# Performance work log

Hardware: AMD Instinct MI355X
Metric: run time of the kernel (lower is better)

Reference implementation:

```python
import jax, jax.numpy as jnp
import numpy as np

B, N, K = 8, 4096, 16
C_IN = 3
MLP = (64, 64, 128)


def _init_conv(key, c_out, c_in):
    kw, kb = jax.random.split(key)
    bound = 1.0 / np.sqrt(c_in)
    W = jax.random.uniform(kw, (c_out, c_in), jnp.float32, -bound, bound)
    b = jax.random.uniform(kb, (c_out,), jnp.float32, -bound, bound)
    return W, b


def setup_inputs() -> dict:
    key = jax.random.key(0)
    k0, k1, k2, k3 = jax.random.split(key, 4)
    xyz = jax.random.normal(k0, (B, C_IN, N), jnp.float32)
    W0, b0 = _init_conv(k1, MLP[0], C_IN)
    W1, b1 = _init_conv(k2, MLP[1], MLP[0])
    W2, b2 = _init_conv(k3, MLP[2], MLP[1])
    return {"xyz": xyz, "W0": W0, "b0": b0, "W1": W1, "b1": b1, "W2": W2, "b2": b2}


def reference(xyz, W0, b0, W1, b1, W2, b2):
    # xyz: [B, 3, N] -> pts: [B, N, 3]
    pts = jnp.transpose(xyz, (0, 2, 1))
    # KNN: squared pairwise distances [B, N, N]
    sq = jnp.sum(pts * pts, axis=-1)  # [B, N]
    d2 = sq[:, :, None] + sq[:, None, :] - 2.0 * jnp.einsum('bnc,bmc->bnm', pts, pts)
    _, idx = jax.lax.top_k(-d2, K)  # [B, N, K] indices of K nearest (incl. self)
    # gather neighbor coords: [B, N, K, 3]
    grouped = jax.vmap(lambda p, i: p[i])(pts, idx)
    # center-relative coordinates
    rel = grouped - pts[:, :, None, :]  # [B, N, K, 3]
    # three 1x1 conv (= per-point linear) + ReLU layers
    h = jax.nn.relu(jnp.einsum('bnkc,oc->bnko', rel, W0) + b0)
    h = jax.nn.relu(jnp.einsum('bnkc,oc->bnko', h, W1) + b1)
    h = jax.nn.relu(jnp.einsum('bnkc,oc->bnko', h, W2) + b2)
    # max over K neighbors -> [B, N, D'] -> [B, D', N]
    out = jnp.max(h, axis=2)
    return jnp.transpose(out, (0, 2, 1))
```

## Files before the change

### kernel.cpp

```cpp
#include <hip/hip_runtime.h>
#include <cstddef>

#define NB   8
#define NPTS 4096
#define KNN  16
#define FCAP 64

typedef _Float16 h2 __attribute__((ext_vector_type(2)));
typedef _Float16 h8 __attribute__((ext_vector_type(8)));
typedef float    f4 __attribute__((ext_vector_type(4)));

static __device__ __forceinline__ h2 pk2(float a, float b) {
    return __builtin_bit_cast(h2, __builtin_amdgcn_cvt_pkrtz(a, b));
}
static __device__ __forceinline__ unsigned bch(h2 v) {
    return __builtin_bit_cast(unsigned, v);
}

#if __has_builtin(__builtin_amdgcn_fmed3f)
static __device__ __forceinline__ float MED3(float a, float b, float c) {
    return __builtin_amdgcn_fmed3f(a, b, c);
}
#else
static __device__ __forceinline__ float MED3(float a, float b, float c) {
    return fmaxf(fminf(a, b), fminf(fmaxf(a, b), c));
}
#endif

static __device__ __forceinline__ float dist2(float4 Q, float4 p) {
    float dot = fmaf(Q.z, p.z, fmaf(Q.y, p.y, Q.x * p.x));
    return fmaf(-2.0f, dot, Q.w + p.w);
}

__global__ __launch_bounds__(256) void prep_kernel(const float* __restrict__ xyz,
                                                   float4* __restrict__ pts4) {
    int i = blockIdx.x * 256 + threadIdx.x;
    int b = i >> 12;
    int n = i & (NPTS - 1);
    const float* base = xyz + (size_t)b * 3 * NPTS;
    float x = base[n];
    float y = base[NPTS + n];
    float z = base[2 * NPTS + n];
    float sq = fmaf(z, z, fmaf(y, y, x * x));
    pts4[i] = make_float4(x, y, z, sq);
}

__global__ __launch_bounds__(1024, 8) void knn_kernel(const float4* __restrict__ pts4,
                                                      int* __restrict__ idxout) {
    __shared__ uint2 Pm[NPTS];
    __shared__ char  sbuf[32768];
    __shared__ float tauv[64];
    __shared__ int   qcnt[64];
    __shared__ unsigned pmaxu, smaxu;

    float*    partials = (float*)sbuf;
    float*    mbuf     = (float*)(sbuf + 16384);
    unsigned* fidx     = (unsigned*)sbuf;
    float*    fdist    = (float*)(sbuf + 16384);

    int tid = threadIdx.x;
    int b   = blockIdx.y;
    const float4* pb = pts4 + (size_t)b * NPTS;

    if (tid == 0) { pmaxu = 0u; smaxu = 0u; }
    __syncthreads();

    {
        float lm = 0.0f, ls = 0.0f;
        for (int j = tid; j < NPTS; j += 1024) {
            float4 p = pb[j];
            lm = fmaxf(lm, fmaxf(fabsf(p.x), fmaxf(fabsf(p.y), fabsf(p.z))));
            ls = fmaxf(ls, p.w);
            h2 lo = { (_Float16)p.x, (_Float16)p.y };
            h2 hi = { (_Float16)p.z, (_Float16)p.w };
            Pm[j].x = bch(lo);
            Pm[j].y = bch(hi);
        }
        atomicMax(&pmaxu, __builtin_bit_cast(unsigned, lm));
        atomicMax(&smaxu, __builtin_bit_cast(unsigned, ls));
    }

    int wave = tid >> 6, lane = tid & 63;
    int qg = wave >> 2;
    int cq = wave & 3;
    int qcol = lane & 15;
    int rg   = lane >> 4;
    int q  = qg * 16 + qcol;
    int nq = (blockIdx.x << 6) + q;
    int cbase = cq * 1024;

    float4 qf = pb[nq];
    float uxf = -2.0f * qf.x, uyf = -2.0f * qf.y, uzf = -2.0f * qf.z;
    _Float16 uxh = (_Float16)uxf, uyh = (_Float16)uyf, uzh = (_Float16)uzf;
    _Float16 uxl = (_Float16)(uxf - (float)uxh);
    _Float16 uyl = (_Float16)(uyf - (float)uyh);
    _Float16 uzl = (_Float16)(uzf - (float)uzh);
    uint4 bu = {0u, 0u, 0u, 0u};
    if (rg == 0) {
        h2 b01 = {uxh, uyh}, b23 = {uzh, (_Float16)1.0f};
        h2 b45 = {uxl, uyl}, b67 = {uzl, (_Float16)0.0f};
        bu.x = bch(b01); bu.y = bch(b23); bu.z = bch(b45); bu.w = bch(b67);
    }
    h8 bq = __builtin_bit_cast(h8, bu);
    __syncthreads();

    {
        float c0 = __builtin_inff(), c1 = c0, c2 = c0, c3 = c0;
#pragma unroll 2
        for (int t = 0; t < 64; ++t) {
            uint4 au = {0u, 0u, 0u, 0u};
            if (rg == 0) {
                uint2 pd = Pm[cbase + t * 16 + qcol];
                au.x = pd.x; au.y = pd.y; au.z = pd.x; au.w = pd.y;
            }
            f4 d = __builtin_amdgcn_mfma_f32_16x16x32_f16(
                __builtin_bit_cast(h8, au), bq, (f4)0.0f, 0, 0, 0);
            float rmin = fminf(fminf(d[0], d[1]), fminf(d[2], d[3]));
            float p0 = c0, p1 = c1, p2 = c2;
            c0 = fminf(p0, rmin);
            c1 = MED3(rmin, p0, c1);
            c2 = MED3(rmin, p1, c2);
            c3 = MED3(rmin, p2, c3);
        }
        int sb = (cq * 4 + rg) * 4;
        partials[(sb + 0) * 64 + q] = c0;
        partials[(sb + 1) * 64 + q] = c1;
        partials[(sb + 2) * 64 + q] = c2;
        partials[(sb + 3) * 64 + q] = c3;
    }
    __syncthreads();

    if (tid < 256) {
        int qq = tid & 63, k = tid >> 6;
        float mb[16];
#pragma unroll
        for (int j = 0; j < 16; ++j) mb[j] = __builtin_inff();
        for (int s = 0; s < 16; ++s) {
            float v = partials[(k * 16 + s) * 64 + qq];
            float prev = mb[0];
            mb[0] = fminf(mb[0], v);
#pragma unroll
            for (int i = 1; i < 16; ++i) {
                float cur = mb[i];
                mb[i] = MED3(v, prev, cur);
                prev = cur;
            }
        }
#pragma unroll
        for (int j = 0; j < 16; ++j) mbuf[(k * 16 + j) * 64 + qq] = mb[j];
    }
    __syncthreads();

    if (tid < 64) {
        float mb[16];
#pragma unroll
        for (int j = 0; j < 16; ++j) mb[j] = __builtin_inff();
        for (int k = 0; k < 4; ++k) {
            for (int j = 0; j < 16; ++j) {
                float v = mbuf[(k * 16 + j) * 64 + tid];
                if (v >= mb[15]) break;
                float prev = mb[0];
                mb[0] = fminf(mb[0], v);
#pragma unroll
                for (int i = 1; i < 16; ++i) {
                    float cur = mb[i];
                    mb[i] = MED3(v, prev, cur);
                    prev = cur;
                }
            }
        }
        float4 q2 = pb[(blockIdx.x << 6) + tid];
        float sumq = fabsf(q2.x) + fabsf(q2.y) + fabsf(q2.z);
        float qn   = sqrtf(q2.w);
        float pmax = __builtin_bit_cast(float, pmaxu);
        float smax = __builtin_bit_cast(float, smaxu);
        const float r11c = 4.8828125e-4f;
        float tau = mb[15];
        float E0  = smax * r11c + 2.0f * sumq * pmax * r11c + 1.0e-3f;
        float rad2 = fmaxf(tau + 2.0f * E0 + q2.w, 0.0f);
        float R   = qn + sqrtf(rad2);
        float Eq  = (R * R + 2.0f * sumq * R) * r11c + 6.0e-4f;
        Eq = fminf(Eq, E0);
        tauv[tid] = tau + 2.0f * Eq;
        qcnt[tid] = 0;
    }
    __syncthreads();

    {
        float tc = tauv[q];
#pragma unroll 2
        for (int t = 0; t < 64; ++t) {
            uint4 au = {0u, 0u, 0u, 0u};
            if (rg == 0) {
                uint2 pd = Pm[cbase + t * 16 + qcol];
                au.x = pd.x; au.y = pd.y; au.z = pd.x; au.w = pd.y;
            }
            f4 d = __builtin_amdgcn_mfma_f32_16x16x32_f16(
                __builtin_bit_cast(h8, au), bq, (f4)0.0f, 0, 0, 0);
            float rmin = fminf(fminf(d[0], d[1]), fminf(d[2], d[3]));
            if (rmin <= tc) {
#pragma unroll
                for (int r = 0; r < 4; ++r) {
                    if (d[r] <= tc) {
                        int pos = atomicAdd(&qcnt[q], 1);
                        if (pos < FCAP) fidx[pos * 64 + q] = (unsigned)(cbase + t * 16 + rg * 4 + r);
                    }
                }
            }
        }
    }
    __syncthreads();

    for (int e = tid; e < FCAP * 64; e += 1024) {
        int j = e >> 6, qq = e & 63;
        int nc = qcnt[qq]; nc = nc > FCAP ? FCAP : nc;
        if (j < nc) {
            float4 Qf = pb[(blockIdx.x << 6) + qq];
            fdist[e] = dist2(Qf, pb[fidx[e]]);
        }
    }
    __syncthreads();

    if (tid < 64) {
        int nqf = (blockIdx.x << 6) + tid;
        float4 Qf = pb[nqf];
        float bd[16]; int bi[16];
#pragma unroll
        for (int j = 0; j < 16; ++j) { bd[j] = __builtin_inff(); bi[j] = 0; }
        int cnt = qcnt[tid];
        if (cnt <= FCAP) {
            for (int j = 0; j < cnt; ++j) {
                float x  = fdist[j * 64 + tid];
                int   xi = (int)fidx[j * 64 + tid];
                if (x < bd[15] || (x == bd[15] && xi < bi[15])) {
#pragma unroll
                    for (int t = 0; t < 16; ++t) {
                        bool c = (x < bd[t]) || (x == bd[t] && xi < bi[t]);
                        float nd = c ? x  : bd[t];
                        int   ni = c ? xi : bi[t];
                        float od = c ? bd[t] : x;
                        int   oi = c ? bi[t] : xi;
                        bd[t] = nd; bi[t] = ni; x = od; xi = oi;
                    }
                }
            }
        } else {
            for (int m = 0; m < NPTS; ++m) {
                float x = dist2(Qf, pb[m]);
                int  xi = m;
                if (x < bd[15] || (x == bd[15] && xi < bi[15])) {
#pragma unroll
                    for (int t = 0; t < 16; ++t) {
                        bool c = (x < bd[t]) || (x == bd[t] && xi < bi[t]);
                        float nd = c ? x  : bd[t];
                        int   ni = c ? xi : bi[t];
                        float od = c ? bd[t] : x;
                        int   oi = c ? bi[t] : xi;
                        bd[t] = nd; bi[t] = ni; x = od; xi = oi;
                    }
                }
            }
        }
        int* op = idxout + ((size_t)b * NPTS + nqf) * KNN;
#pragma unroll
        for (int j = 0; j < 16; ++j) op[j] = bi[j];
    }
}

__global__ __launch_bounds__(256, 2) void mlp_kernel(
    const float4* __restrict__ pts4, const int* __restrict__ idxin,
    const float* __restrict__ W0, const float* __restrict__ b0,
    const float* __restrict__ W1, const float* __restrict__ b1,
    const float* __restrict__ W2, const float* __restrict__ b2,
    float* __restrict__ out) {

    int tid  = threadIdx.x;
    int wave = tid >> 6, lane = tid & 63;
    int g = lane >> 4, i = lane & 15;

    h2 w0x[8], w0y[8], w0z[8], w0b[8];
#pragma unroll
    for (int s = 0; s < 2; ++s)
#pragma unroll
        for (int v = 0; v < 4; ++v) {
            int c0 = 32 * s + 8 * g + 2 * v;
            w0x[s * 4 + v] = pk2(W0[c0 * 3 + 0], W0[c0 * 3 + 3]);
            w0y[s * 4 + v] = pk2(W0[c0 * 3 + 1], W0[c0 * 3 + 4]);
            w0z[s * 4 + v] = pk2(W0[c0 * 3 + 2], W0[c0 * 3 + 5]);
            w0b[s * 4 + v] = pk2(b0[c0], b0[c0 + 1]);
        }
    h2 b1p[8];
#pragma unroll
    for (int s = 0; s < 2; ++s)
#pragma unroll
        for (int v = 0; v < 4; ++v) {
            int c0 = 32 * s + 16 * (v >> 1) + 4 * g + 2 * (v & 1);
            b1p[s * 4 + v] = pk2(b1[c0], b1[c0 + 1]);
        }
    h8 wf1[4][2];
#pragma unroll
    for (int t = 0; t < 4; ++t)
#pragma unroll
        for (int s = 0; s < 2; ++s) {
            const float* p = W1 + (16 * t + i) * 64 + 32 * s + 8 * g;
            h8 f;
#pragma unroll
            for (int j = 0; j < 8; ++j) f[j] = (_Float16)p[j];
            wf1[t][s] = f;
        }
    h8 wf2[8][2];
#pragma unroll
    for (int t = 0; t < 8; ++t)
#pragma unroll
        for (int s = 0; s < 2; ++s) {
            const float* p = W2 + (16 * t + i) * 64;
            h8 f;
#pragma unroll
            for (int j = 0; j < 8; ++j) {
                int vc = 32 * s + 16 * (j >> 2) + 4 * g + (j & 3);
                f[j] = (_Float16)p[vc];
            }
            wf2[t][s] = f;
        }

    int gw = blockIdx.x * 4 + wave;
    int b  = gw >> 8;
    int n0 = (gw & 255) * 16;

    const float4* pb = pts4 + (size_t)b * NPTS;
    float4 q = pb[n0 + i];
    const int* ip = idxin + ((size_t)b * NPTS + n0 + i) * KNN;

    float mx[8][4];
#pragma unroll
    for (int t = 0; t < 8; ++t)
#pragma unroll
        for (int r = 0; r < 4; ++r) mx[t][r] = -3.4e38f;

    for (int it = 0; it < KNN; ++it) {
        int mi = ip[it];
        float4 p = pb[mi];
        float rx = p.x - q.x, ry = p.y - q.y, rz = p.z - q.z;
        h2 rxx = pk2(rx, rx), ryy = pk2(ry, ry), rzz = pk2(rz, rz);

        h8 h0f[2];
#pragma unroll
        for (int s = 0; s < 2; ++s)
#pragma unroll
            for (int v = 0; v < 4; ++v) {
                h2 hh = __builtin_elementwise_fma(w0z[s * 4 + v], rzz,
                         __builtin_elementwise_fma(w0y[s * 4 + v], ryy,
                          __builtin_elementwise_fma(w0x[s * 4 + v], rxx, w0b[s * 4 + v])));
                hh = __builtin_elementwise_max(hh, (h2)(_Float16)0.0f);
                h0f[s][2 * v]     = hh.x;
                h0f[s][2 * v + 1] = hh.y;
            }

        f4 d1[4];
#pragma unroll
        for (int t = 0; t < 4; ++t) {
            d1[t] = (f4)0.0f;
#pragma unroll
            for (int s = 0; s < 2; ++s)
                d1[t] = __builtin_amdgcn_mfma_f32_16x16x32_f16(wf1[t][s], h0f[s], d1[t], 0, 0, 0);
        }

        h8 h1f[2];
#pragma unroll
        for (int s = 0; s < 2; ++s)
#pragma unroll
            for (int v = 0; v < 4; ++v) {
                int t = 2 * s + (v >> 1), r0 = 2 * (v & 1);
                h2 w = pk2(d1[t][r0], d1[t][r0 + 1]);
                w = w + b1p[s * 4 + v];
                w = __builtin_elementwise_max(w, (h2)(_Float16)0.0f);
                h1f[s][2 * v]     = w.x;
                h1f[s][2 * v + 1] = w.y;
            }

#pragma unroll
        for (int t = 0; t < 8; ++t) {
            f4 d2 = (f4)0.0f;
#pragma unroll
            for (int s = 0; s < 2; ++s)
                d2 = __builtin_amdgcn_mfma_f32_16x16x32_f16(wf2[t][s], h1f[s], d2, 0, 0, 0);
#pragma unroll
            for (int r = 0; r < 4; ++r) mx[t][r] = fmaxf(mx[t][r], d2[r]);
        }
    }

    size_t ob = (size_t)b * 128 * NPTS + n0 + i;
#pragma unroll
    for (int t = 0; t < 8; ++t)
#pragma unroll
        for (int r = 0; r < 4; ++r) {
            int chn = 16 * t + 4 * g + r;
            float v = fmaxf(mx[t][r] + b2[chn], 0.0f);
            out[ob + (size_t)chn * NPTS] = v;
        }
}

extern "C" void kernel_launch(void* const* d_in, const int* in_sizes, int n_in,
                              void* d_out, int out_size, void* d_ws, size_t ws_size,
                              hipStream_t stream) {
    (void)in_sizes; (void)n_in; (void)out_size; (void)ws_size;
    const float* xyz = (const float*)d_in[0];
    const float* W0  = (const float*)d_in[1];
    const float* b0  = (const float*)d_in[2];
    const float* W1  = (const float*)d_in[3];
    const float* b1  = (const float*)d_in[4];
    const float* W2  = (const float*)d_in[5];
    const float* b2  = (const float*)d_in[6];
    float* out = (float*)d_out;

    char* ws = (char*)d_ws;
    float4* pts4 = (float4*)ws;
    int*    idxb = (int*)(ws + (size_t)NB * NPTS * sizeof(float4));

    prep_kernel<<<dim3(NB * NPTS / 256), dim3(256), 0, stream>>>(xyz, pts4);
    knn_kernel<<<dim3(NPTS / 64, NB), dim3(1024), 0, stream>>>(pts4, idxb);
    mlp_kernel<<<dim3(512), dim3(256), 0, stream>>>(
        pts4, idxb, W0, b0, W1, b1, W2, b2, out);
}
```

Measured before the change: 118.3 us.

## Switch KNN distance MFMA from 16x16x32 to 32x32x16 tiles

The KNN distance passes now use the 32x32x16 f16 MFMA instead of 16x16x32. Each wave covers 32 queries and 512 candidates in 16 iterations, and the wave-to-query/candidate mapping changes to 2 query groups by 8 candidate chunks. The goal is fewer MFMA issues and fewer loop iterations per candidate. In exchange, each lane carries 16 output registers, runs a wider min-reduction tree, and the filter pass's unrolled atomic checks grow from 4 to 16 per tile, which may raise register pressure and branch divergence.

```diff
diff --git a/kernel.cpp b/kernel.cpp
--- a/kernel.cpp
+++ b/kernel.cpp
@@ -9,6 +9,7 @@
 typedef _Float16 h2 __attribute__((ext_vector_type(2)));
 typedef _Float16 h8 __attribute__((ext_vector_type(8)));
 typedef float    f4 __attribute__((ext_vector_type(4)));
+typedef float    f16f __attribute__((ext_vector_type(16)));
 
 static __device__ __forceinline__ h2 pk2(float a, float b) {
     return __builtin_bit_cast(h2, __builtin_amdgcn_cvt_pkrtz(a, b));
@@ -81,13 +82,13 @@
     }
 
     int wave = tid >> 6, lane = tid & 63;
-    int qg = wave >> 2;
-    int cq = wave & 3;
-    int qcol = lane & 15;
-    int rg   = lane >> 4;
-    int q  = qg * 16 + qcol;
+    int g  = wave >> 3;
+    int c  = wave & 7;
+    int col = lane & 31;
+    int hl  = lane >> 5;
+    int q  = g * 32 + col;
     int nq = (blockIdx.x << 6) + q;
-    int cbase = cq * 1024;
+    int cbase = c * 512;
 
     float4 qf = pb[nq];
     float uxf = -2.0f * qf.x, uyf = -2.0f * qf.y, uzf = -2.0f * qf.z;
@@ -96,7 +97,7 @@
     _Float16 uyl = (_Float16)(uyf - (float)uyh);
     _Float16 uzl = (_Float16)(uzf - (float)uzh);
     uint4 bu = {0u, 0u, 0u, 0u};
-    if (rg == 0) {
+    if (hl == 0) {
         h2 b01 = {uxh, uyh}, b23 = {uzh, (_Float16)1.0f};
         h2 b45 = {uxl, uyl}, b67 = {uzl, (_Float16)0.0f};
         bu.x = bch(b01); bu.y = bch(b23); bu.z = bch(b45); bu.w = bch(b67);
@@ -107,22 +108,28 @@
     {
         float c0 = __builtin_inff(), c1 = c0, c2 = c0, c3 = c0;
 #pragma unroll 2
-        for (int t = 0; t < 64; ++t) {
+        for (int t = 0; t < 16; ++t) {
             uint4 au = {0u, 0u, 0u, 0u};
-            if (rg == 0) {
-                uint2 pd = Pm[cbase + t * 16 + qcol];
+            if (hl == 0) {
+                uint2 pd = Pm[cbase + t * 32 + col];
                 au.x = pd.x; au.y = pd.y; au.z = pd.x; au.w = pd.y;
             }
-            f4 d = __builtin_amdgcn_mfma_f32_16x16x32_f16(
-                __builtin_bit_cast(h8, au), bq, (f4)0.0f, 0, 0, 0);
-            float rmin = fminf(fminf(d[0], d[1]), fminf(d[2], d[3]));
+            f16f d = __builtin_amdgcn_mfma_f32_32x32x16_f16(
+                __builtin_bit_cast(h8, au), bq, (f16f)0.0f, 0, 0, 0);
+            float a0 = fminf(d[0], d[1]),   a1 = fminf(d[2], d[3]);
+            float a2 = fminf(d[4], d[5]),   a3 = fminf(d[6], d[7]);
+            float a4 = fminf(d[8], d[9]),   a5 = fminf(d[10], d[11]);
+            float a6 = fminf(d[12], d[13]), a7 = fminf(d[14], d[15]);
+            float b0 = fminf(a0, a1), b1 = fminf(a2, a3);
+            float b2 = fminf(a4, a5), b3 = fminf(a6, a7);
+            float rmin = fminf(fminf(b0, b1), fminf(b2, b3));
             float p0 = c0, p1 = c1, p2 = c2;
             c0 = fminf(p0, rmin);
             c1 = MED3(rmin, p0, c1);
             c2 = MED3(rmin, p1, c2);
             c3 = MED3(rmin, p2, c3);
         }
-        int sb = (cq * 4 + rg) * 4;
+        int sb = (c * 2 + hl) * 4;
         partials[(sb + 0) * 64 + q] = c0;
         partials[(sb + 1) * 64 + q] = c1;
         partials[(sb + 2) * 64 + q] = c2;
@@ -188,23 +195,22 @@
 
     {
         float tc = tauv[q];
-#pragma unroll 2
-        for (int t = 0; t < 64; ++t) {
+#pragma unroll 1
+        for (int t = 0; t < 16; ++t) {
             uint4 au = {0u, 0u, 0u, 0u};
-            if (rg == 0) {
-                uint2 pd = Pm[cbase + t * 16 + qcol];
+            if (hl == 0) {
+                uint2 pd = Pm[cbase + t * 32 + col];
                 au.x = pd.x; au.y = pd.y; au.z = pd.x; au.w = pd.y;
             }
-            f4 d = __builtin_amdgcn_mfma_f32_16x16x32_f16(
-                __builtin_bit_cast(h8, au), bq, (f4)0.0f, 0, 0, 0);
-            float rmin = fminf(fminf(d[0], d[1]), fminf(d[2], d[3]));
-            if (rmin <= tc) {
-#pragma unroll
-                for (int r = 0; r < 4; ++r) {
-                    if (d[r] <= tc) {
-                        int pos = atomicAdd(&qcnt[q], 1);
-                        if (pos < FCAP) fidx[pos * 64 + q] = (unsigned)(cbase + t * 16 + rg * 4 + r);
-                    }
+            f16f d = __builtin_amdgcn_mfma_f32_32x32x16_f16(
+                __builtin_bit_cast(h8, au), bq, (f16f)0.0f, 0, 0, 0);
+#pragma unroll
+            for (int r = 0; r < 16; ++r) {
+                if (d[r] <= tc) {
+                    int pos = atomicAdd(&qcnt[q], 1);
+                    if (pos < FCAP)
+                        fidx[pos * 64 + q] =
+                            (unsigned)(cbase + t * 32 + (r & 3) + 8 * (r >> 2) + 4 * hl);
                 }
             }
         }
@@ -235,11 +241,11 @@
                 if (x < bd[15] || (x == bd[15] && xi < bi[15])) {
 #pragma unroll
                     for (int t = 0; t < 16; ++t) {
-                        bool c = (x < bd[t]) || (x == bd[t] && xi < bi[t]);
-                        float nd = c ? x  : bd[t];
-                        int   ni = c ? xi : bi[t];
-                        float od = c ? bd[t] : x;
-                        int   oi = c ? bi[t] : xi;
+                        bool cc = (x < bd[t]) || (x == bd[t] && xi < bi[t]);
+                        float nd = cc ? x  : bd[t];
+                        int   ni = cc ? xi : bi[t];
+                        float od = cc ? bd[t] : x;
+                        int   oi = cc ? bi[t] : xi;
                         bd[t] = nd; bi[t] = ni; x = od; xi = oi;
                     }
                 }
@@ -251,11 +257,11 @@
                 if (x < bd[15] || (x == bd[15] && xi < bi[15])) {
 #pragma unroll
                     for (int t = 0; t < 16; ++t) {
-                        bool c = (x < bd[t]) || (x == bd[t] && xi < bi[t]);
-                        float nd = c ? x  : bd[t];
-                        int   ni = c ? xi : bi[t];
-                        float od = c ? bd[t] : x;
-                        int   oi = c ? bi[t] : xi;
+                        bool cc = (x < bd[t]) || (x == bd[t] && xi < bi[t]);
+                        float nd = cc ? x  : bd[t];
+                        int   ni = cc ? xi : bi[t];
+                        float od = cc ? bd[t] : x;
+                        int   oi = cc ? bi[t] : xi;
                         bd[t] = nd; bi[t] = ni; x = od; xi = oi;
                     }
                 }
```

Measured after the change: 106.9 us. -9.6%, faster.
